# Optimization experiments

Measured on AMD Instinct MI355X. Metric: run time of the kernel, lower is better.

## Reference

```python
import jax, jax.numpy as jnp
import numpy as np

C_PER_GROUP = 16
T_ITERS = 5
EPS = 1e-5


def setup_inputs() -> dict:
    key = jax.random.key(0)
    k1, = jax.random.split(key, 1)
    N, C, H, W = 32, 256, 64, 64
    x = jax.random.normal(k1, (N, C, H, W), dtype=jnp.float32)
    return {
        "x": x,
        "sw_mean_weight": jnp.ones((2,), jnp.float32),
        "sw_var_weight": jnp.ones((2,), jnp.float32),
        "weight": jnp.ones((C,), jnp.float32),
        "bias": jnp.zeros((C,), jnp.float32),
    }


def reference(x, sw_mean_weight, sw_var_weight, weight, bias):
    N, C, H, W = x.shape
    c = C_PER_GROUP
    g = C // c
    HW = H * W
    NHW = N * HW

    # --- BW (batch whitening) stats over all N,H,W per group (world_size=1) ---
    # torch: x.transpose(0,1).view(g, c, N*H*W)
    xt = jnp.transpose(x, (1, 0, 2, 3)).reshape(g, c, NHW)
    mean_bn = jnp.mean(xt, axis=-1, keepdims=True)              # (g, c, 1)
    xc = xt - mean_bn
    cov_bn = jnp.einsum('gci,gdi->gcd', xc, xc) / NHW           # (g, c, c)

    # broadcast BN stats to (N*g, ...)
    mean_bn_b = jnp.broadcast_to(mean_bn[None], (N, g, c, 1)).reshape(N * g, c, 1)
    cov_bn_b = jnp.broadcast_to(cov_bn[None], (N, g, c, c)).reshape(N * g, c, c)

    # --- IW (instance whitening) stats per (sample, group) ---
    in_data = x.reshape(N * g, c, HW)
    mean_in = jnp.mean(in_data, axis=-1, keepdims=True)         # (N*g, c, 1)
    x_in = in_data - mean_in
    cov_in = jnp.einsum('bci,bdi->bcd', x_in, x_in) / HW        # (N*g, c, c)

    eye = jnp.eye(c, dtype=x.dtype)

    # --- switchable mixing (sw_type = 2: BW + IW) ---
    mw = jax.nn.softmax(sw_mean_weight)
    vw = jax.nn.softmax(sw_var_weight)
    mean = mw[0] * mean_bn_b + mw[1] * mean_in                  # (N*g, c, 1)
    cov = vw[0] * cov_bn_b + vw[1] * cov_in + EPS * eye         # (N*g, c, c)

    # --- Newton-Schulz iterative whitening ---
    trace = jnp.trace(cov, axis1=-2, axis2=-1)[:, None, None]   # (N*g, 1, 1)
    rTr = 1.0 / trace
    cov_N = cov * rTr
    P = jnp.broadcast_to(eye, cov.shape)
    for _ in range(T_ITERS):
        P3 = jnp.matmul(jnp.matmul(P, P), P)
        P = 1.5 * P - 0.5 * jnp.matmul(P3, cov_N)
    wm = P * jnp.sqrt(rTr)                                      # (N*g, c, c)

    x_hat = jnp.matmul(wm, in_data - mean).reshape(N, C, H, W)
    x_hat = x_hat * weight[None, :, None, None] + bias[None, :, None, None]
    return x_hat
```

## Files before the change

### kernel.cpp

```cpp
#include <hip/hip_runtime.h>

#define HWSZ 4096
#define NTRI 136
#define NSTAT 152
#define NINST 512
#define GCNT 16
#define EPSW 1e-5f

typedef float v2f __attribute__((ext_vector_type(2)));
typedef float v4f __attribute__((ext_vector_type(4)));

__global__ __launch_bounds__(256, 2) void k_inst_stats(const float* __restrict__ x,
                                                       float* __restrict__ inst_stats) {
  const int b = blockIdx.x;
  const int t = threadIdx.x;
  const v2f* xb = (const v2f*)x + (size_t)b * 16 * 2048;

  float s1[16];
  float s2[NTRI];
#pragma unroll
  for (int i = 0; i < 16; ++i) s1[i] = 0.f;
#pragma unroll
  for (int i = 0; i < NTRI; ++i) s2[i] = 0.f;

#pragma unroll 1
  for (int k = 0; k < 8; ++k) {
    const int f = t + k * 256;
    v2f v[16];
#pragma unroll
    for (int d = 0; d < 16; ++d) v[d] = xb[d * 2048 + f];
#pragma unroll
    for (int c = 0; c < 16; ++c) s1[c] += v[c].x + v[c].y;
    int tri = 0;
#pragma unroll
    for (int c = 0; c < 16; ++c) {
#pragma unroll
      for (int d = c; d < 16; ++d) {
        s2[tri] += v[c].x * v[d].x + v[c].y * v[d].y;
        ++tri;
      }
    }
  }

  __shared__ float red[4 * NSTAT];
  const int lane = t & 63;
  const int wv = t >> 6;
#pragma unroll
  for (int q = 0; q < 16; ++q) {
    float v = s1[q];
#pragma unroll
    for (int off = 32; off > 0; off >>= 1) v += __shfl_down(v, off);
    if (lane == 0) red[wv * NSTAT + q] = v;
  }
#pragma unroll
  for (int q = 0; q < NTRI; ++q) {
    float v = s2[q];
#pragma unroll
    for (int off = 32; off > 0; off >>= 1) v += __shfl_down(v, off);
    if (lane == 0) red[wv * NSTAT + 16 + q] = v;
  }
  __syncthreads();
  if (t < NSTAT) {
    inst_stats[(size_t)b * NSTAT + t] =
        red[t] + red[NSTAT + t] + red[2 * NSTAT + t] + red[3 * NSTAT + t];
  }
}

__global__ __launch_bounds__(192) void k_group(const float* __restrict__ inst_stats,
                                               float* __restrict__ grp_stats) {
  const int g = blockIdx.x;
  const int t = threadIdx.x;
  if (t < NSTAT) {
    float s = 0.f;
    for (int n = 0; n < 32; ++n) s += inst_stats[(size_t)(n * GCNT + g) * NSTAT + t];
    grp_stats[(size_t)g * NSTAT + t] = s;
  }
}

__global__ __launch_bounds__(256) void k_newton(const float* __restrict__ inst_stats,
                                                const float* __restrict__ grp_stats,
                                                const float* __restrict__ swm,
                                                const float* __restrict__ swv,
                                                const float* __restrict__ weight,
                                                const float* __restrict__ bias,
                                                float* __restrict__ apply_wm,
                                                float* __restrict__ apply_ofs) {
  const int b = blockIdx.x;
  const int g = b & 15;
  const int t = threadIdx.x;
  const int r = t >> 4;
  const int c = t & 15;

  __shared__ float P[256], Qm[256], Rm[256], CN[256], Wl[256];
  __shared__ float Mm[16], Mi[16], Mb[16];

  float a0 = swm[0], a1 = swm[1];
  float mx = fmaxf(a0, a1);
  float e0 = expf(a0 - mx), e1 = expf(a1 - mx);
  const float mw0 = e0 / (e0 + e1), mw1 = e1 / (e0 + e1);
  a0 = swv[0]; a1 = swv[1];
  mx = fmaxf(a0, a1);
  e0 = expf(a0 - mx); e1 = expf(a1 - mx);
  const float vw0 = e0 / (e0 + e1), vw1 = e1 / (e0 + e1);

  const float inv_hw = 1.0f / (float)HWSZ;
  const float inv_nhw = 1.0f / (32.0f * (float)HWSZ);

  if (t < 16) {
    const float mi = inst_stats[(size_t)b * NSTAT + t] * inv_hw;
    const float mb = grp_stats[(size_t)g * NSTAT + t] * inv_nhw;
    Mi[t] = mi;
    Mb[t] = mb;
    Mm[t] = mw0 * mb + mw1 * mi;
  }
  __syncthreads();

  const int cmin = (r < c) ? r : c;
  const int cmax = (r < c) ? c : r;
  const int tri = 15 * cmin - (cmin * (cmin - 1)) / 2 + cmax + 16;
  const float cin = inst_stats[(size_t)b * NSTAT + tri] * inv_hw - Mi[r] * Mi[c];
  const float cbn = grp_stats[(size_t)g * NSTAT + tri] * inv_nhw - Mb[r] * Mb[c];
  float cov = vw0 * cbn + vw1 * cin + ((r == c) ? EPSW : 0.0f);

  Qm[t] = cov;
  __syncthreads();
  float trace = 0.f;
#pragma unroll
  for (int i = 0; i < 16; ++i) trace += Qm[i * 16 + i];
  const float rTr = 1.0f / trace;

  CN[t] = cov * rTr;
  P[t] = (r == c) ? 1.0f : 0.0f;
  __syncthreads();

  for (int it = 0; it < 5; ++it) {
    float q = 0.f;
#pragma unroll
    for (int k = 0; k < 16; ++k) q += P[r * 16 + k] * P[k * 16 + c];
    Qm[t] = q;
    __syncthreads();
    float rr = 0.f;
#pragma unroll
    for (int k = 0; k < 16; ++k) rr += Qm[r * 16 + k] * P[k * 16 + c];
    Rm[t] = rr;
    __syncthreads();
    float tt = 0.f;
#pragma unroll
    for (int k = 0; k < 16; ++k) tt += Rm[r * 16 + k] * CN[k * 16 + c];
    const float np = 1.5f * P[t] - 0.5f * tt;
    __syncthreads();
    P[t] = np;
    __syncthreads();
  }

  const float sr = sqrtf(rTr);
  const float wel = P[t] * sr * weight[g * 16 + r];
  Wl[t] = wel;
  apply_wm[(size_t)b * 256 + t] = wel;
  __syncthreads();
  if (t < 16) {
    float acc = 0.f;
#pragma unroll
    for (int d = 0; d < 16; ++d) acc += Wl[t * 16 + d] * Mm[d];
    apply_ofs[(size_t)b * 16 + t] = bias[g * 16 + t] - acc;
  }
}

__global__ __launch_bounds__(256, 4) void k_apply(const float* __restrict__ x,
                                                  const float* __restrict__ apply_wm,
                                                  const float* __restrict__ apply_ofs,
                                                  float* __restrict__ y) {
  const int bb = blockIdx.x;
  const int b = bb >> 2;
  const int chunk = bb & 3;
  const int t = threadIdx.x;

  __shared__ float Wl[256];
  __shared__ float Ol[16];
  Wl[t] = apply_wm[(size_t)b * 256 + t];
  if (t < 16) Ol[t] = apply_ofs[(size_t)b * 16 + t];
  __syncthreads();

  const v4f* xb = (const v4f*)x + (size_t)b * 16 * 1024;
  v4f* yb = (v4f*)y + (size_t)b * 16 * 1024;
  const int f = chunk * 256 + t;

  v4f v[16];
#pragma unroll
  for (int d = 0; d < 16; ++d) v[d] = xb[d * 1024 + f];

#pragma unroll
  for (int cch = 0; cch < 16; ++cch) {
    v4f acc = Ol[cch];
#pragma unroll
    for (int d = 0; d < 16; ++d) acc += Wl[cch * 16 + d] * v[d];
    yb[cch * 1024 + f] = acc;
  }
}

extern "C" void kernel_launch(void* const* d_in, const int* in_sizes, int n_in,
                              void* d_out, int out_size, void* d_ws, size_t ws_size,
                              hipStream_t stream) {
  const float* x = (const float*)d_in[0];
  const float* swm = (const float*)d_in[1];
  const float* swv = (const float*)d_in[2];
  const float* weight = (const float*)d_in[3];
  const float* bias = (const float*)d_in[4];
  float* out = (float*)d_out;

  float* ws = (float*)d_ws;
  float* inst = ws;
  float* grp = inst + (size_t)NINST * NSTAT;
  float* awm = grp + (size_t)GCNT * NSTAT;
  float* aofs = awm + (size_t)NINST * 256;

  k_inst_stats<<<NINST, 256, 0, stream>>>(x, inst);
  k_group<<<GCNT, 192, 0, stream>>>(inst, grp);
  k_newton<<<NINST, 256, 0, stream>>>(inst, grp, swm, swv, weight, bias, awm, aofs);
  k_apply<<<NINST * 4, 256, 0, stream>>>(x, awm, aofs, out);
}
```

Baseline: 302.8 us.

## Split instance-stats covariance across two blocks per instance to cut registers

The instance statistics kernel now launches two blocks per (sample, group). One block computes the means and the first 58 covariance entries (rows 0-3), and the other computes the remaining 78 entries from channels 4-15. This shrinks each thread's accumulator array so launch bounds can request 4 blocks per SM, raising occupancy. In exchange, the second block re-reads 12 of the 16 channels, adding global traffic on the stats pass.

```diff
diff --git a/kernel.cpp b/kernel.cpp
--- a/kernel.cpp
+++ b/kernel.cpp
@@ -10,59 +10,98 @@
 typedef float v2f __attribute__((ext_vector_type(2)));
 typedef float v4f __attribute__((ext_vector_type(4)));
 
-__global__ __launch_bounds__(256, 2) void k_inst_stats(const float* __restrict__ x,
+__global__ __launch_bounds__(256, 4) void k_inst_stats(const float* __restrict__ x,
                                                        float* __restrict__ inst_stats) {
-  const int b = blockIdx.x;
-  const int t = threadIdx.x;
-  const v2f* xb = (const v2f*)x + (size_t)b * 16 * 2048;
-
-  float s1[16];
-  float s2[NTRI];
-#pragma unroll
-  for (int i = 0; i < 16; ++i) s1[i] = 0.f;
-#pragma unroll
-  for (int i = 0; i < NTRI; ++i) s2[i] = 0.f;
-
-#pragma unroll 1
-  for (int k = 0; k < 8; ++k) {
-    const int f = t + k * 256;
-    v2f v[16];
-#pragma unroll
-    for (int d = 0; d < 16; ++d) v[d] = xb[d * 2048 + f];
-#pragma unroll
-    for (int c = 0; c < 16; ++c) s1[c] += v[c].x + v[c].y;
-    int tri = 0;
-#pragma unroll
-    for (int c = 0; c < 16; ++c) {
-#pragma unroll
-      for (int d = c; d < 16; ++d) {
-        s2[tri] += v[c].x * v[d].x + v[c].y * v[d].y;
-        ++tri;
-      }
-    }
-  }
-
-  __shared__ float red[4 * NSTAT];
+  const int bb = blockIdx.x;
+  const int b = bb >> 1;
+  const int half = bb & 1;
+  const int t = threadIdx.x;
   const int lane = t & 63;
   const int wv = t >> 6;
-#pragma unroll
-  for (int q = 0; q < 16; ++q) {
-    float v = s1[q];
-#pragma unroll
-    for (int off = 32; off > 0; off >>= 1) v += __shfl_down(v, off);
-    if (lane == 0) red[wv * NSTAT + q] = v;
-  }
-#pragma unroll
-  for (int q = 0; q < NTRI; ++q) {
-    float v = s2[q];
-#pragma unroll
-    for (int off = 32; off > 0; off >>= 1) v += __shfl_down(v, off);
-    if (lane == 0) red[wv * NSTAT + 16 + q] = v;
-  }
-  __syncthreads();
-  if (t < NSTAT) {
-    inst_stats[(size_t)b * NSTAT + t] =
-        red[t] + red[NSTAT + t] + red[2 * NSTAT + t] + red[3 * NSTAT + t];
+  const v2f* xb = (const v2f*)x + (size_t)b * 16 * 2048;
+
+  __shared__ float red[4 * 78];
+
+  if (half == 0) {
+    float s1[16];
+    float s2[58];
+#pragma unroll
+    for (int i = 0; i < 16; ++i) s1[i] = 0.f;
+#pragma unroll
+    for (int i = 0; i < 58; ++i) s2[i] = 0.f;
+
+#pragma unroll 1
+    for (int k = 0; k < 8; ++k) {
+      const int f = t + k * 256;
+      v2f v[16];
+#pragma unroll
+      for (int d = 0; d < 16; ++d) v[d] = xb[d * 2048 + f];
+#pragma unroll
+      for (int c = 0; c < 16; ++c) s1[c] += v[c].x + v[c].y;
+      int tri = 0;
+#pragma unroll
+      for (int c = 0; c < 4; ++c) {
+#pragma unroll
+        for (int d = c; d < 16; ++d) {
+          s2[tri] += v[c].x * v[d].x + v[c].y * v[d].y;
+          ++tri;
+        }
+      }
+    }
+
+#pragma unroll
+    for (int q = 0; q < 16; ++q) {
+      float v = s1[q];
+#pragma unroll
+      for (int off = 32; off > 0; off >>= 1) v += __shfl_down(v, off);
+      if (lane == 0) red[wv * 78 + q] = v;
+    }
+#pragma unroll
+    for (int q = 0; q < 58; ++q) {
+      float v = s2[q];
+#pragma unroll
+      for (int off = 32; off > 0; off >>= 1) v += __shfl_down(v, off);
+      if (lane == 0) red[wv * 78 + 16 + q] = v;
+    }
+    __syncthreads();
+    if (t < 74) {
+      inst_stats[(size_t)b * NSTAT + t] =
+          red[t] + red[78 + t] + red[156 + t] + red[234 + t];
+    }
+  } else {
+    float s2[78];
+#pragma unroll
+    for (int i = 0; i < 78; ++i) s2[i] = 0.f;
+
+#pragma unroll 1
+    for (int k = 0; k < 8; ++k) {
+      const int f = t + k * 256;
+      v2f v[12];
+#pragma unroll
+      for (int d = 0; d < 12; ++d) v[d] = xb[(d + 4) * 2048 + f];
+      int tri = 0;
+#pragma unroll
+      for (int c = 0; c < 12; ++c) {
+#pragma unroll
+        for (int d = c; d < 12; ++d) {
+          s2[tri] += v[c].x * v[d].x + v[c].y * v[d].y;
+          ++tri;
+        }
+      }
+    }
+
+#pragma unroll
+    for (int q = 0; q < 78; ++q) {
+      float v = s2[q];
+#pragma unroll
+      for (int off = 32; off > 0; off >>= 1) v += __shfl_down(v, off);
+      if (lane == 0) red[wv * 78 + q] = v;
+    }
+    __syncthreads();
+    if (t < 78) {
+      inst_stats[(size_t)b * NSTAT + 74 + t] =
+          red[t] + red[78 + t] + red[156 + t] + red[234 + t];
+    }
   }
 }
 
@@ -214,7 +253,7 @@
   float* awm = grp + (size_t)GCNT * NSTAT;
   float* aofs = awm + (size_t)NINST * 256;
 
-  k_inst_stats<<<NINST, 256, 0, stream>>>(x, inst);
+  k_inst_stats<<<NINST * 2, 256, 0, stream>>>(x, inst);
   k_group<<<GCNT, 192, 0, stream>>>(inst, grp);
   k_newton<<<NINST, 256, 0, stream>>>(inst, grp, swm, swv, weight, bias, awm, aofs);
   k_apply<<<NINST * 4, 256, 0, stream>>>(x, awm, aofs, out);
```

After: 317.8 us. 1.05x slower.

## Double-buffer stats loads via async global-to-LDS copies and fold group reduction into newton

Applied to the files above, without the earlier changes.

The instance-statistics kernel now stages 16-channel chunks of x into a double-buffered LDS region using global_load_lds, so the next chunk loads while the current one is reduced. This is meant to hide global memory latency. Separately, the group-sum kernel is removed and each newton block recomputes its group's sums from the instance stats, which saves one launch at the cost of redundant reads. The 64 KB LDS buffer may limit occupancy, and the extra __syncthreads in each iteration adds some stall.

```diff
diff --git a/kernel.cpp b/kernel.cpp
--- a/kernel.cpp
+++ b/kernel.cpp
@@ -1,4 +1,5 @@
 #include <hip/hip_runtime.h>
+#include <stdint.h>
 
 #define HWSZ 4096
 #define NTRI 136
@@ -6,15 +7,38 @@
 #define NINST 512
 #define GCNT 16
 #define EPSW 1e-5f
+#define CHUNK 512
+#define NCHUNK 8
 
 typedef float v2f __attribute__((ext_vector_type(2)));
 typedef float v4f __attribute__((ext_vector_type(4)));
+
+typedef __attribute__((address_space(3))) float lds_f;
+typedef const __attribute__((address_space(1))) float glb_f;
+
+__device__ __forceinline__ void stage_chunk(const float* __restrict__ xb,
+                                            float* bufp, int wv, int lane, int ck) {
+#pragma unroll
+  for (int ii = 0; ii < 8; ++ii) {
+    const int d = wv * 4 + (ii >> 1);
+    const int q = ii & 1;
+    __builtin_amdgcn_global_load_lds(
+        (glb_f*)(xb + (size_t)d * HWSZ + (size_t)ck * CHUNK + q * 256 + lane * 4),
+        (lds_f*)(bufp + d * CHUNK + q * 256), 16, 0, 0);
+  }
+}
 
 __global__ __launch_bounds__(256, 2) void k_inst_stats(const float* __restrict__ x,
                                                        float* __restrict__ inst_stats) {
   const int b = blockIdx.x;
   const int t = threadIdx.x;
-  const v2f* xb = (const v2f*)x + (size_t)b * 16 * 2048;
+  const int lane = t & 63;
+  const int wv = t >> 6;
+
+  __shared__ float buf[2][16 * CHUNK];
+  __shared__ float red[4 * NSTAT];
+
+  const float* xb = x + (size_t)b * 16 * HWSZ;
 
   float s1[16];
   float s2[NTRI];
@@ -23,12 +47,16 @@
 #pragma unroll
   for (int i = 0; i < NTRI; ++i) s2[i] = 0.f;
 
+  stage_chunk(xb, &buf[0][0], wv, lane, 0);
+  __syncthreads();
+
 #pragma unroll 1
-  for (int k = 0; k < 8; ++k) {
-    const int f = t + k * 256;
+  for (int ck = 0; ck < NCHUNK; ++ck) {
+    if (ck + 1 < NCHUNK) stage_chunk(xb, &buf[(ck + 1) & 1][0], wv, lane, ck + 1);
+    const float* bc = &buf[ck & 1][0];
     v2f v[16];
 #pragma unroll
-    for (int d = 0; d < 16; ++d) v[d] = xb[d * 2048 + f];
+    for (int d = 0; d < 16; ++d) v[d] = *(const v2f*)&bc[d * CHUNK + 2 * t];
 #pragma unroll
     for (int c = 0; c < 16; ++c) s1[c] += v[c].x + v[c].y;
     int tri = 0;
@@ -40,11 +68,9 @@
         ++tri;
       }
     }
-  }
-
-  __shared__ float red[4 * NSTAT];
-  const int lane = t & 63;
-  const int wv = t >> 6;
+    __syncthreads();
+  }
+
 #pragma unroll
   for (int q = 0; q < 16; ++q) {
     float v = s1[q];
@@ -66,19 +92,7 @@
   }
 }
 
-__global__ __launch_bounds__(192) void k_group(const float* __restrict__ inst_stats,
-                                               float* __restrict__ grp_stats) {
-  const int g = blockIdx.x;
-  const int t = threadIdx.x;
-  if (t < NSTAT) {
-    float s = 0.f;
-    for (int n = 0; n < 32; ++n) s += inst_stats[(size_t)(n * GCNT + g) * NSTAT + t];
-    grp_stats[(size_t)g * NSTAT + t] = s;
-  }
-}
-
 __global__ __launch_bounds__(256) void k_newton(const float* __restrict__ inst_stats,
-                                                const float* __restrict__ grp_stats,
                                                 const float* __restrict__ swm,
                                                 const float* __restrict__ swv,
                                                 const float* __restrict__ weight,
@@ -93,6 +107,14 @@
 
   __shared__ float P[256], Qm[256], Rm[256], CN[256], Wl[256];
   __shared__ float Mm[16], Mi[16], Mb[16];
+  __shared__ float Gs[NSTAT];
+
+  if (t < NSTAT) {
+    float s = 0.f;
+#pragma unroll 8
+    for (int n = 0; n < 32; ++n) s += inst_stats[(size_t)(n * GCNT + g) * NSTAT + t];
+    Gs[t] = s;
+  }
 
   float a0 = swm[0], a1 = swm[1];
   float mx = fmaxf(a0, a1);
@@ -106,9 +128,11 @@
   const float inv_hw = 1.0f / (float)HWSZ;
   const float inv_nhw = 1.0f / (32.0f * (float)HWSZ);
 
+  __syncthreads();
+
   if (t < 16) {
     const float mi = inst_stats[(size_t)b * NSTAT + t] * inv_hw;
-    const float mb = grp_stats[(size_t)g * NSTAT + t] * inv_nhw;
+    const float mb = Gs[t] * inv_nhw;
     Mi[t] = mi;
     Mb[t] = mb;
     Mm[t] = mw0 * mb + mw1 * mi;
@@ -119,7 +143,7 @@
   const int cmax = (r < c) ? c : r;
   const int tri = 15 * cmin - (cmin * (cmin - 1)) / 2 + cmax + 16;
   const float cin = inst_stats[(size_t)b * NSTAT + tri] * inv_hw - Mi[r] * Mi[c];
-  const float cbn = grp_stats[(size_t)g * NSTAT + tri] * inv_nhw - Mb[r] * Mb[c];
+  const float cbn = Gs[tri] * inv_nhw - Mb[r] * Mb[c];
   float cov = vw0 * cbn + vw1 * cin + ((r == c) ? EPSW : 0.0f);
 
   Qm[t] = cov;
@@ -210,12 +234,10 @@
 
   float* ws = (float*)d_ws;
   float* inst = ws;
-  float* grp = inst + (size_t)NINST * NSTAT;
-  float* awm = grp + (size_t)GCNT * NSTAT;
+  float* awm = inst + (size_t)NINST * NSTAT;
   float* aofs = awm + (size_t)NINST * 256;
 
   k_inst_stats<<<NINST, 256, 0, stream>>>(x, inst);
-  k_group<<<GCNT, 192, 0, stream>>>(inst, grp);
-  k_newton<<<NINST, 256, 0, stream>>>(inst, grp, swm, swv, weight, bias, awm, aofs);
+  k_newton<<<NINST, 256, 0, stream>>>(inst, swm, swv, weight, bias, awm, aofs);
   k_apply<<<NINST * 4, 256, 0, stream>>>(x, awm, aofs, out);
 }
```

Result: no change. 297.5 us (-1.7%).
